# Kernel tuning notes

Measured on AMD Instinct MI355X. Metric: run time of the kernel, lower is better.

## Reference

```python
import jax, jax.numpy as jnp
import numpy as np

POOLED_H = 7
POOLED_W = 7
SPATIAL_SCALE = 0.25
S = 2  # sampling_ratio (static grid per bin)
ALIGNED_OFFSET = 0.5  # aligned=True


def setup_inputs() -> dict:
    key = jax.random.key(0)
    k1, k2, k3, k4 = jax.random.split(key, 4)
    B, C, H, W = 2, 256, 200, 200
    K = 1000
    x = jax.random.normal(k1, (B, C, H, W), dtype=jnp.float32)
    img_w = W / SPATIAL_SCALE  # 800.0, image-space coords
    img_h = H / SPATIAL_SCALE
    bidx = jax.random.randint(k2, (K,), 0, B).astype(jnp.float32)
    xy1 = jax.random.uniform(k3, (K, 2), dtype=jnp.float32) * jnp.array([img_w * 0.7, img_h * 0.7], jnp.float32)
    wh = jax.random.uniform(k4, (K, 2), dtype=jnp.float32) * jnp.array([img_w * 0.3, img_h * 0.3], jnp.float32) + 1.0
    rois = jnp.concatenate([bidx[:, None], xy1[:, 0:1], xy1[:, 1:2],
                            xy1[:, 0:1] + wh[:, 0:1], xy1[:, 1:2] + wh[:, 1:2]], axis=1)
    return {"x": x, "rois": rois}


def _axis(start, bin_size, pooled, limit):
    """Per-axis sample coords + bilinear corner indices/weights.
    start, bin_size: [K]. Returns low, high [K, pooled*S] int32 and
    w_low, w_high [K, pooled*S] float (validity folded into weights)."""
    p = jnp.arange(pooled, dtype=start.dtype)
    s = (jnp.arange(S, dtype=start.dtype) + 0.5) / S
    coord = start[:, None, None] + (p[None, :, None] + s[None, None, :]) * bin_size[:, None, None]
    coord = coord.reshape(coord.shape[0], pooled * S)  # [K, pooled*S]
    valid = ((coord >= -1.0) & (coord <= limit)).astype(coord.dtype)
    c = jnp.maximum(coord, 0.0)
    low0 = jnp.floor(c).astype(jnp.int32)
    cap = low0 >= limit - 1
    low = jnp.where(cap, limit - 1, low0)
    high = jnp.where(cap, limit - 1, low0 + 1)
    c = jnp.where(cap, low.astype(c.dtype), c)
    l = c - low.astype(c.dtype)
    h = 1.0 - l
    return low, high, h * valid, l * valid


def _roi_align(x, rois):
    B, C, H, W = x.shape
    bidx = rois[:, 0].astype(jnp.int32)
    start_w = rois[:, 1] * SPATIAL_SCALE - ALIGNED_OFFSET
    start_h = rois[:, 2] * SPATIAL_SCALE - ALIGNED_OFFSET
    end_w = rois[:, 3] * SPATIAL_SCALE - ALIGNED_OFFSET
    end_h = rois[:, 4] * SPATIAL_SCALE - ALIGNED_OFFSET
    bin_h = (end_h - start_h) / POOLED_H
    bin_w = (end_w - start_w) / POOLED_W
    yl, yh, wy0, wy1 = _axis(start_h, bin_h, POOLED_H, H)  # [K, PH*S]
    xl, xh, wx0, wx1 = _axis(start_w, bin_w, POOLED_W, W)  # [K, PW*S]
    xt = x.reshape(B, C, H * W).transpose(0, 2, 1)  # [B, HW, C]

    def gather(yi, xi):
        pos = yi[:, :, None] * W + xi[:, None, :]          # [K, NY, NX]
        return xt[bidx[:, None, None], pos, :]             # [K, NY, NX, C]

    out = (wy0[:, :, None, None] * wx0[:, None, :, None] * gather(yl, xl)
         + wy0[:, :, None, None] * wx1[:, None, :, None] * gather(yl, xh)
         + wy1[:, :, None, None] * wx0[:, None, :, None] * gather(yh, xl)
         + wy1[:, :, None, None] * wx1[:, None, :, None] * gather(yh, xh))
    K = rois.shape[0]
    # average over the SxS sample grid inside each bin
    out = out.reshape(K, POOLED_H, S, POOLED_W, S, C).sum(axis=(2, 4)) / float(S * S)
    return out.transpose(0, 3, 1, 2)  # [K, C, PH, PW]


def reference(x, rois):
    return _roi_align(x, rois)
```

## Files before the change

### kernel.cpp

```cpp
#include <hip/hip_runtime.h>
#include <hip/hip_bf16.h>


#define PH 7
#define PW 7
#define SCALE 0.25f
#define C_ 256
#define CH_ 128
#define H_ 200
#define W_ 200
#define HW_ (H_ * W_)

typedef float f32x4 __attribute__((ext_vector_type(4)));

__global__ void __launch_bounds__(512)
transpose_kernel(const float* __restrict__ x, __hip_bfloat16* __restrict__ xt) {
    __shared__ float tile[64][65];
    int hw0 = blockIdx.x * 64;
    int c0  = blockIdx.y * 64;
    int b   = blockIdx.z;
    int tx = threadIdx.x;
    int ty = threadIdx.y;
    const float* xb = x + (size_t)b * C_ * HW_;
#pragma unroll
    for (int j = 0; j < 8; ++j) {
        int cl = ty + 8 * j;
        tile[cl][tx] = __builtin_nontemporal_load(&xb[(size_t)(c0 + cl) * HW_ + hw0 + tx]);
    }
    __syncthreads();
    __hip_bfloat16* xtb = xt + (size_t)b * HW_ * C_;
#pragma unroll
    for (int j = 0; j < 8; ++j) {
        int rl = ty + 8 * j;
        float v = tile[tx][rl];
        xtb[(size_t)(hw0 + rl) * C_ + c0 + tx] = __float2bfloat16(v);
    }
}

__global__ void __launch_bounds__(1024)
sort_rois_kernel(const float* __restrict__ rois, int K, int* __restrict__ perm) {
    __shared__ int s[1024];
    int t = threadIdx.x;
    int key;
    if (t < K) {
        const float* r = rois + (size_t)t * 5;
        int b = (int)r[0];
        float yc = (r[2] + r[4]) * (0.5f * SCALE);
        int yq = min(max((int)yc, 0), 511);
        key = ((b * 512 + yq) << 12) | t;
    } else {
        key = 0x7FFFFFFF;
    }
    s[t] = key;
    __syncthreads();
    for (int k2 = 2; k2 <= 1024; k2 <<= 1) {
        for (int j = k2 >> 1; j > 0; j >>= 1) {
            int ixj = t ^ j;
            if (ixj > t) {
                int a = s[t], bv = s[ixj];
                bool up = ((t & k2) == 0);
                if ((a > bv) == up) { s[t] = bv; s[ixj] = a; }
            }
            __syncthreads();
        }
    }
    if (t < K) perm[t] = s[t] & 0xFFF;
}

__global__ void identity_perm_kernel(int K, int* __restrict__ perm) {
    int i = blockIdx.x * blockDim.x + threadIdx.x;
    if (i < K) perm[i] = i;
}

__global__ void __launch_bounds__(512)
roi_main(const __hip_bfloat16* __restrict__ xt, const float* __restrict__ rois,
         const int* __restrict__ perm, float* __restrict__ out, int K) {
    __shared__ float s_out[CH_ * 49];
    __shared__ int   s_ylo[14], s_yhi[14], s_xlo[14], s_xhi[14];
    __shared__ float s_wy0[14], s_wy1[14], s_wx0[14], s_wx1[14];
    __shared__ int   s_b;

    int nwg = gridDim.x;
    int q = nwg >> 3, rr = nwg & 7;
    int xcd = blockIdx.x & 7, pos = blockIdx.x >> 3;
    int logical = (xcd < rr ? xcd * (q + 1) : rr * (q + 1) + (xcd - rr) * q) + pos;

    int k     = perm[logical >> 1];
    int chalf = logical & 1;
    int t = threadIdx.x;
    const float* r = rois + (size_t)k * 5;
    if (t == 0) s_b = (int)r[0];
    if (t < 28) {
        bool isy = t < 14;
        int i = isy ? t : t - 14;
        float start = (isy ? r[2] : r[1]) * SCALE - 0.5f;
        float end   = (isy ? r[4] : r[3]) * SCALE - 0.5f;
        float bin = (end - start) * (1.0f / 7.0f);
        int limit = isy ? H_ : W_;
        float pp   = (float)(i >> 1);
        float soff = (i & 1) ? 0.75f : 0.25f;
        float coord = fmaf(pp + soff, bin, start);
        float valid = (coord >= -1.0f && coord <= (float)limit) ? 1.0f : 0.0f;
        float cc = fmaxf(coord, 0.0f);
        int low0 = (int)floorf(cc);
        bool cap = low0 >= limit - 1;
        int lo = cap ? limit - 1 : low0;
        int hi = cap ? limit - 1 : low0 + 1;
        cc = cap ? (float)lo : cc;
        float l = cc - (float)lo;
        float w1 = l * valid, w0 = (1.0f - l) * valid;
        if (isy) { s_ylo[i] = lo; s_yhi[i] = hi; s_wy0[i] = w0; s_wy1[i] = w1; }
        else     { s_xlo[i] = lo; s_xhi[i] = hi; s_wx0[i] = w0; s_wx1[i] = w1; }
    }
    __syncthreads();

    int cg = t & 15;
    int pq = t >> 4;

    const __hip_bfloat16* xb = xt + (size_t)s_b * HW_ * C_ + chalf * CH_ + cg * 8;

    for (int p = pq; p < 49; p += 32) {
        int ph = p / 7;
        int pw = p - ph * 7;
        float acc[8];
#pragma unroll
        for (int j = 0; j < 8; ++j) acc[j] = 0.0f;

#pragma unroll
        for (int sy = 0; sy < 2; ++sy) {
            int ys = 2 * ph + sy;
            int yl = s_ylo[ys], yh = s_yhi[ys];
            float wy0 = s_wy0[ys], wy1 = s_wy1[ys];
#pragma unroll
            for (int sx = 0; sx < 2; ++sx) {
                int xs = 2 * pw + sx;
                int xl = s_xlo[xs], xh = s_xhi[xs];
                float wx0 = s_wx0[xs], wx1 = s_wx1[xs];
                float w00 = wy0 * wx0, w01 = wy0 * wx1;
                float w10 = wy1 * wx0, w11 = wy1 * wx1;
                uint4 v00 = *(const uint4*)(xb + ((size_t)(yl * W_ + xl) << 8));
                uint4 v01 = *(const uint4*)(xb + ((size_t)(yl * W_ + xh) << 8));
                uint4 v10 = *(const uint4*)(xb + ((size_t)(yh * W_ + xl) << 8));
                uint4 v11 = *(const uint4*)(xb + ((size_t)(yh * W_ + xh) << 8));
                const unsigned* a00 = (const unsigned*)&v00;
                const unsigned* a01 = (const unsigned*)&v01;
                const unsigned* a10 = (const unsigned*)&v10;
                const unsigned* a11 = (const unsigned*)&v11;
#pragma unroll
                for (int w = 0; w < 4; ++w) {
                    float f00l = __uint_as_float(a00[w] << 16);
                    float f00h = __uint_as_float(a00[w] & 0xffff0000u);
                    float f01l = __uint_as_float(a01[w] << 16);
                    float f01h = __uint_as_float(a01[w] & 0xffff0000u);
                    float f10l = __uint_as_float(a10[w] << 16);
                    float f10h = __uint_as_float(a10[w] & 0xffff0000u);
                    float f11l = __uint_as_float(a11[w] << 16);
                    float f11h = __uint_as_float(a11[w] & 0xffff0000u);
                    acc[2 * w]     = fmaf(w00, f00l, acc[2 * w]);
                    acc[2 * w]     = fmaf(w01, f01l, acc[2 * w]);
                    acc[2 * w]     = fmaf(w10, f10l, acc[2 * w]);
                    acc[2 * w]     = fmaf(w11, f11l, acc[2 * w]);
                    acc[2 * w + 1] = fmaf(w00, f00h, acc[2 * w + 1]);
                    acc[2 * w + 1] = fmaf(w01, f01h, acc[2 * w + 1]);
                    acc[2 * w + 1] = fmaf(w10, f10h, acc[2 * w + 1]);
                    acc[2 * w + 1] = fmaf(w11, f11h, acc[2 * w + 1]);
                }
            }
        }
#pragma unroll
        for (int j = 0; j < 8; ++j)
            s_out[(cg * 8 + j) * 49 + p] = acc[j] * 0.25f;
    }
    __syncthreads();

    const f32x4* sv = (const f32x4*)s_out;
    f32x4* ov = (f32x4*)(out + ((size_t)k * C_ + chalf * CH_) * 49);
    for (int i = t; i < (CH_ * 49) / 4; i += 512)
        __builtin_nontemporal_store(sv[i], &ov[i]);
}

__device__ __forceinline__ void axis_sample(float coord, int limit,
                                            int& lo, int& hi,
                                            float& w0, float& w1) {
    float fl = (float)limit;
    float valid = (coord >= -1.0f && coord <= fl) ? 1.0f : 0.0f;
    float c = fmaxf(coord, 0.0f);
    int low0 = (int)floorf(c);
    bool cap = low0 >= limit - 1;
    lo = cap ? limit - 1 : low0;
    hi = cap ? limit - 1 : low0 + 1;
    c = cap ? (float)lo : c;
    float l = c - (float)lo;
    w1 = l * valid;
    w0 = (1.0f - l) * valid;
}

__global__ void __launch_bounds__(256)
roi_align_fallback(const float* __restrict__ x, const float* __restrict__ rois,
                   float* __restrict__ out, int total) {
    int idx = blockIdx.x * blockDim.x + threadIdx.x;
    if (idx >= total) return;
    int pw = idx % PW;
    int ph = (idx / PW) % PH;
    int c  = (idx / (PW * PH)) % C_;
    int k  = idx / (PW * PH * C_);
    const float* r = rois + (size_t)k * 5;
    int b = (int)r[0];
    float start_w = r[1] * SCALE - 0.5f;
    float start_h = r[2] * SCALE - 0.5f;
    float bin_w = (r[3] * SCALE - 0.5f - start_w) / (float)PW;
    float bin_h = (r[4] * SCALE - 0.5f - start_h) / (float)PH;
    const float* xp = x + ((size_t)b * C_ + c) * (size_t)HW_;
    float acc = 0.0f;
#pragma unroll
    for (int sy = 0; sy < 2; ++sy) {
        float yc = start_h + ((float)ph + (sy + 0.5f) * 0.5f) * bin_h;
        int yl, yh; float wy0, wy1;
        axis_sample(yc, H_, yl, yh, wy0, wy1);
        const float* row0 = xp + (size_t)yl * W_;
        const float* row1 = xp + (size_t)yh * W_;
#pragma unroll
        for (int sx = 0; sx < 2; ++sx) {
            float xc = start_w + ((float)pw + (sx + 0.5f) * 0.5f) * bin_w;
            int xl, xh; float wx0, wx1;
            axis_sample(xc, W_, xl, xh, wx0, wx1);
            acc += wy0 * (wx0 * row0[xl] + wx1 * row0[xh])
                 + wy1 * (wx0 * row1[xl] + wx1 * row1[xh]);
        }
    }
    out[idx] = acc * 0.25f;
}

extern "C" void kernel_launch(void* const* d_in, const int* in_sizes, int n_in,
                              void* d_out, int out_size, void* d_ws, size_t ws_size,
                              hipStream_t stream) {
    const float* x    = (const float*)d_in[0];
    const float* rois = (const float*)d_in[1];
    float* out = (float*)d_out;
    int K = in_sizes[1] / 5;

    size_t xtbytes = (size_t)2 * HW_ * C_ * sizeof(__hip_bfloat16);
    size_t need = xtbytes + 4096 * sizeof(int);
    if (ws_size >= need && K <= 4096) {
        __hip_bfloat16* xt = (__hip_bfloat16*)d_ws;
        int* perm = (int*)((char*)d_ws + xtbytes);
        dim3 tgrid(HW_ / 64, C_ / 64, 2);
        dim3 tblock(64, 8);
        transpose_kernel<<<tgrid, tblock, 0, stream>>>(x, xt);
        if (K <= 1024)
            sort_rois_kernel<<<1, 1024, 0, stream>>>(rois, K, perm);
        else
            identity_perm_kernel<<<(K + 255) / 256, 256, 0, stream>>>(K, perm);
        roi_main<<<K * 2, 512, 0, stream>>>(xt, rois, perm, out, K);
    } else {
        int total = K * C_ * PH * PW;
        roi_align_fallback<<<(total + 255) / 256, 256, 0, stream>>>(x, rois, out, total);
    }
}
```

Baseline: 59.97 us.

## Fuse ROI sort into transpose kernel, remap XCD blocks, split x-corners across lanes

The ROI sort moves into an extra block of the transpose kernel, so one launch goes away. roi_main gets a new block-to-ROI mapping that sends each channel half to its own group of XCDs, which should improve L2 locality. Each sample's two x-corners are now split across lane pairs and combined with a cross-lane shuffle, doubling thread parallelism per bin, and the 0.25 averaging factor is folded into the y weights. The costs are one extra shuffle per output plus a serial bitonic sort that runs inside one block of the transpose grid.

```diff
diff --git a/kernel.cpp b/kernel.cpp
--- a/kernel.cpp
+++ b/kernel.cpp
@@ -14,13 +14,53 @@
 typedef float f32x4 __attribute__((ext_vector_type(4)));
 
 __global__ void __launch_bounds__(512)
-transpose_kernel(const float* __restrict__ x, __hip_bfloat16* __restrict__ xt) {
+transpose_sort_kernel(const float* __restrict__ x, __hip_bfloat16* __restrict__ xt,
+                      const float* __restrict__ rois, int K, int mode,
+                      int* __restrict__ perm) {
     __shared__ float tile[64][65];
-    int hw0 = blockIdx.x * 64;
+    __shared__ int s[1024];
+    int bx = blockIdx.x;
+    int tx = threadIdx.x;
+    int ty = threadIdx.y;
+    int t = ty * 64 + tx;
+
+    if (bx == gridDim.x - 1) {
+        if (blockIdx.y != 0 || blockIdx.z != 0) return;
+        if (mode == 1) {
+            for (int i = t; i < 1024; i += 512) {
+                int key;
+                if (i < K) {
+                    const float* r = rois + (size_t)i * 5;
+                    int b = (int)r[0];
+                    float yc = (r[2] + r[4]) * (0.5f * SCALE);
+                    int yq = min(max((int)yc, 0), 511);
+                    key = ((b * 512 + yq) << 12) | i;
+                } else {
+                    key = 0x7FFFFFFF;
+                }
+                s[i] = key;
+            }
+            __syncthreads();
+            for (int k2 = 2; k2 <= 1024; k2 <<= 1) {
+                for (int j = k2 >> 1; j > 0; j >>= 1) {
+                    int i = ((t & ~(j - 1)) << 1) | (t & (j - 1));
+                    int l = i | j;
+                    int a = s[i], b = s[l];
+                    bool up = ((i & k2) == 0);
+                    if ((a > b) == up) { s[i] = b; s[l] = a; }
+                    __syncthreads();
+                }
+            }
+            for (int i = t; i < K; i += 512) perm[i] = s[i] & 0xFFF;
+        } else {
+            for (int i = t; i < K; i += 512) perm[i] = i;
+        }
+        return;
+    }
+
+    int hw0 = bx * 64;
     int c0  = blockIdx.y * 64;
     int b   = blockIdx.z;
-    int tx = threadIdx.x;
-    int ty = threadIdx.y;
     const float* xb = x + (size_t)b * C_ * HW_;
 #pragma unroll
     for (int j = 0; j < 8; ++j) {
@@ -37,56 +77,30 @@
     }
 }
 
-__global__ void __launch_bounds__(1024)
-sort_rois_kernel(const float* __restrict__ rois, int K, int* __restrict__ perm) {
-    __shared__ int s[1024];
-    int t = threadIdx.x;
-    int key;
-    if (t < K) {
-        const float* r = rois + (size_t)t * 5;
-        int b = (int)r[0];
-        float yc = (r[2] + r[4]) * (0.5f * SCALE);
-        int yq = min(max((int)yc, 0), 511);
-        key = ((b * 512 + yq) << 12) | t;
-    } else {
-        key = 0x7FFFFFFF;
-    }
-    s[t] = key;
-    __syncthreads();
-    for (int k2 = 2; k2 <= 1024; k2 <<= 1) {
-        for (int j = k2 >> 1; j > 0; j >>= 1) {
-            int ixj = t ^ j;
-            if (ixj > t) {
-                int a = s[t], bv = s[ixj];
-                bool up = ((t & k2) == 0);
-                if ((a > bv) == up) { s[t] = bv; s[ixj] = a; }
-            }
-            __syncthreads();
-        }
-    }
-    if (t < K) perm[t] = s[t] & 0xFFF;
-}
-
-__global__ void identity_perm_kernel(int K, int* __restrict__ perm) {
-    int i = blockIdx.x * blockDim.x + threadIdx.x;
-    if (i < K) perm[i] = i;
-}
-
 __global__ void __launch_bounds__(512)
 roi_main(const __hip_bfloat16* __restrict__ xt, const float* __restrict__ rois,
-         const int* __restrict__ perm, float* __restrict__ out, int K) {
+         const int* __restrict__ perm, float* __restrict__ out, int K, int mode) {
     __shared__ float s_out[CH_ * 49];
-    __shared__ int   s_ylo[14], s_yhi[14], s_xlo[14], s_xhi[14];
+    __shared__ int   s_ylo[14], s_yhi[14], s_xlo[14];
     __shared__ float s_wy0[14], s_wy1[14], s_wx0[14], s_wx1[14];
     __shared__ int   s_b;
 
-    int nwg = gridDim.x;
-    int q = nwg >> 3, rr = nwg & 7;
-    int xcd = blockIdx.x & 7, pos = blockIdx.x >> 3;
-    int logical = (xcd < rr ? xcd * (q + 1) : rr * (q + 1) + (xcd - rr) * q) + pos;
-
-    int k     = perm[logical >> 1];
-    int chalf = logical & 1;
+    int k, chalf;
+    if (mode == 1) {
+        int xcd  = blockIdx.x & 7;
+        int pos  = blockIdx.x >> 3;
+        chalf    = xcd >> 2;
+        int rank = (xcd & 3) * (K >> 2) + pos;
+        k = perm[rank];
+    } else {
+        int nwg = gridDim.x;
+        int q = nwg >> 3, rr = nwg & 7;
+        int xcd = blockIdx.x & 7, pos = blockIdx.x >> 3;
+        int logical = (xcd < rr ? xcd * (q + 1) : rr * (q + 1) + (xcd - rr) * q) + pos;
+        k = perm[logical >> 1];
+        chalf = logical & 1;
+    }
+
     int t = threadIdx.x;
     const float* r = rois + (size_t)k * 5;
     if (t == 0) s_b = (int)r[0];
@@ -109,17 +123,23 @@
         cc = cap ? (float)lo : cc;
         float l = cc - (float)lo;
         float w1 = l * valid, w0 = (1.0f - l) * valid;
-        if (isy) { s_ylo[i] = lo; s_yhi[i] = hi; s_wy0[i] = w0; s_wy1[i] = w1; }
-        else     { s_xlo[i] = lo; s_xhi[i] = hi; s_wx0[i] = w0; s_wx1[i] = w1; }
+        if (isy) {
+            s_ylo[i] = lo; s_yhi[i] = hi;
+            s_wy0[i] = w0 * 0.25f; s_wy1[i] = w1 * 0.25f;
+        } else {
+            s_xlo[i] = lo;
+            s_wx0[i] = w0; s_wx1[i] = w1;
+        }
     }
     __syncthreads();
 
-    int cg = t & 15;
-    int pq = t >> 4;
+    int cg    = t & 15;
+    int xc    = (t >> 4) & 1;
+    int pslot = t >> 5;
 
     const __hip_bfloat16* xb = xt + (size_t)s_b * HW_ * C_ + chalf * CH_ + cg * 8;
 
-    for (int p = pq; p < 49; p += 32) {
+    for (int p = pslot; p < 49; p += 16) {
         int ph = p / 7;
         int pw = p - ph * 7;
         float acc[8];
@@ -134,42 +154,31 @@
 #pragma unroll
             for (int sx = 0; sx < 2; ++sx) {
                 int xs = 2 * pw + sx;
-                int xl = s_xlo[xs], xh = s_xhi[xs];
-                float wx0 = s_wx0[xs], wx1 = s_wx1[xs];
-                float w00 = wy0 * wx0, w01 = wy0 * wx1;
-                float w10 = wy1 * wx0, w11 = wy1 * wx1;
-                uint4 v00 = *(const uint4*)(xb + ((size_t)(yl * W_ + xl) << 8));
-                uint4 v01 = *(const uint4*)(xb + ((size_t)(yl * W_ + xh) << 8));
-                uint4 v10 = *(const uint4*)(xb + ((size_t)(yh * W_ + xl) << 8));
-                uint4 v11 = *(const uint4*)(xb + ((size_t)(yh * W_ + xh) << 8));
-                const unsigned* a00 = (const unsigned*)&v00;
-                const unsigned* a01 = (const unsigned*)&v01;
-                const unsigned* a10 = (const unsigned*)&v10;
-                const unsigned* a11 = (const unsigned*)&v11;
+                int xi = s_xlo[xs] + xc;
+                float wxm = xc ? s_wx1[xs] : s_wx0[xs];
+                float wl = wy0 * wxm, wh = wy1 * wxm;
+                uint4 vlo = *(const uint4*)(xb + ((size_t)(yl * W_ + xi) << 8));
+                uint4 vhi = *(const uint4*)(xb + ((size_t)(yh * W_ + xi) << 8));
+                const unsigned* alo = (const unsigned*)&vlo;
+                const unsigned* ahi = (const unsigned*)&vhi;
 #pragma unroll
                 for (int w = 0; w < 4; ++w) {
-                    float f00l = __uint_as_float(a00[w] << 16);
-                    float f00h = __uint_as_float(a00[w] & 0xffff0000u);
-                    float f01l = __uint_as_float(a01[w] << 16);
-                    float f01h = __uint_as_float(a01[w] & 0xffff0000u);
-                    float f10l = __uint_as_float(a10[w] << 16);
-                    float f10h = __uint_as_float(a10[w] & 0xffff0000u);
-                    float f11l = __uint_as_float(a11[w] << 16);
-                    float f11h = __uint_as_float(a11[w] & 0xffff0000u);
-                    acc[2 * w]     = fmaf(w00, f00l, acc[2 * w]);
-                    acc[2 * w]     = fmaf(w01, f01l, acc[2 * w]);
-                    acc[2 * w]     = fmaf(w10, f10l, acc[2 * w]);
-                    acc[2 * w]     = fmaf(w11, f11l, acc[2 * w]);
-                    acc[2 * w + 1] = fmaf(w00, f00h, acc[2 * w + 1]);
-                    acc[2 * w + 1] = fmaf(w01, f01h, acc[2 * w + 1]);
-                    acc[2 * w + 1] = fmaf(w10, f10h, acc[2 * w + 1]);
-                    acc[2 * w + 1] = fmaf(w11, f11h, acc[2 * w + 1]);
+                    float flo0 = __uint_as_float(alo[w] << 16);
+                    float flo1 = __uint_as_float(alo[w] & 0xffff0000u);
+                    float fhi0 = __uint_as_float(ahi[w] << 16);
+                    float fhi1 = __uint_as_float(ahi[w] & 0xffff0000u);
+                    acc[2 * w]     = fmaf(wl, flo0, acc[2 * w]);
+                    acc[2 * w]     = fmaf(wh, fhi0, acc[2 * w]);
+                    acc[2 * w + 1] = fmaf(wl, flo1, acc[2 * w + 1]);
+                    acc[2 * w + 1] = fmaf(wh, fhi1, acc[2 * w + 1]);
                 }
             }
         }
 #pragma unroll
-        for (int j = 0; j < 8; ++j)
-            s_out[(cg * 8 + j) * 49 + p] = acc[j] * 0.25f;
+        for (int j = 0; j < 8; ++j) {
+            float v = acc[j] + __shfl_xor(acc[j], 16, 64);
+            if (xc == 0) s_out[(cg * 8 + j) * 49 + p] = v;
+        }
     }
     __syncthreads();
 
@@ -221,9 +230,9 @@
         const float* row1 = xp + (size_t)yh * W_;
 #pragma unroll
         for (int sx = 0; sx < 2; ++sx) {
-            float xc = start_w + ((float)pw + (sx + 0.5f) * 0.5f) * bin_w;
+            float xc2 = start_w + ((float)pw + (sx + 0.5f) * 0.5f) * bin_w;
             int xl, xh; float wx0, wx1;
-            axis_sample(xc, W_, xl, xh, wx0, wx1);
+            axis_sample(xc2, W_, xl, xh, wx0, wx1);
             acc += wy0 * (wx0 * row0[xl] + wx1 * row0[xh])
                  + wy1 * (wx0 * row1[xl] + wx1 * row1[xh]);
         }
@@ -241,17 +250,14 @@
 
     size_t xtbytes = (size_t)2 * HW_ * C_ * sizeof(__hip_bfloat16);
     size_t need = xtbytes + 4096 * sizeof(int);
-    if (ws_size >= need && K <= 4096) {
+    if (ws_size >= need && K <= 4096 && K >= 8) {
         __hip_bfloat16* xt = (__hip_bfloat16*)d_ws;
         int* perm = (int*)((char*)d_ws + xtbytes);
-        dim3 tgrid(HW_ / 64, C_ / 64, 2);
+        int mode = (K % 4 == 0 && K <= 1024) ? 1 : 0;
+        dim3 tgrid(HW_ / 64 + 1, C_ / 64, 2);
         dim3 tblock(64, 8);
-        transpose_kernel<<<tgrid, tblock, 0, stream>>>(x, xt);
-        if (K <= 1024)
-            sort_rois_kernel<<<1, 1024, 0, stream>>>(rois, K, perm);
-        else
-            identity_perm_kernel<<<(K + 255) / 256, 256, 0, stream>>>(K, perm);
-        roi_main<<<K * 2, 512, 0, stream>>>(xt, rois, perm, out, K);
+        transpose_sort_kernel<<<tgrid, tblock, 0, stream>>>(x, xt, rois, K, mode, perm);
+        roi_main<<<K * 2, 512, 0, stream>>>(xt, rois, perm, out, K, mode);
     } else {
         int total = K * C_ * PH * PW;
         roi_align_fallback<<<(total + 255) / 256, 256, 0, stream>>>(x, rois, out, total);
```

Result: faster. 51.27 us (-14.5%).
